# Performance work log

Hardware: AMD Instinct MI355X
Metric: run time of the kernel (lower is better)

## Reference

```python
import jax, jax.numpy as jnp
import numpy as np

N = 100000      # nodes
E = 1600000     # edges (avg degree 16)
D_IN, D_H, D_OUT = 128, 128, 64


def setup_inputs() -> dict:
    key = jax.random.key(0)
    ks = jax.random.split(key, 8)
    x = jax.random.normal(ks[0], (N, D_IN), dtype=jnp.float32)
    edge_index = jax.random.randint(ks[1], (2, E), 0, N, dtype=jnp.int64)

    def lin(k, fi, fo):
        s = float(1.0 / np.sqrt(fi))
        return jax.random.normal(k, (fi, fo), dtype=jnp.float32) * s

    return {
        "x": x,
        "edge_index": edge_index,
        "W0": lin(ks[2], D_IN, D_H),  "b0": jnp.zeros((D_H,), jnp.float32),
        "W1": lin(ks[3], D_H, D_H),   "b1": jnp.zeros((D_H,), jnp.float32),
        "W2": lin(ks[4], D_H, D_OUT), "b2": jnp.zeros((D_OUT,), jnp.float32),
    }


def gcn_conv(x, W, b, src, dst, deg_inv_sqrt):
    # PyG GCNConv: h = x W; out = D^-1/2 (A + I) D^-1/2 h + b
    h = x @ W                                             # [N, F_out]
    coef = deg_inv_sqrt[src] * deg_inv_sqrt[dst]          # [E]
    msg = h[src] * coef[:, None]                          # [E, F_out] gather
    out = jax.ops.segment_sum(msg, dst, num_segments=N)   # scatter-add
    out = out + (deg_inv_sqrt * deg_inv_sqrt)[:, None] * h  # self-loops
    return out + b


def reference(x, edge_index, W0, b0, W1, b1, W2, b2):
    src, dst = edge_index[0], edge_index[1]
    # degree includes the self-loop (+1), matching add_self_loops fill_value=1
    deg = jnp.zeros((N,), x.dtype).at[dst].add(1.0) + 1.0
    dis = jax.lax.rsqrt(deg)

    h = jax.nn.relu(gcn_conv(x, W0, b0, src, dst, dis))   # dropout: eval mode -> identity
    h = jax.nn.relu(gcn_conv(h, W1, b1, src, dst, dis))
    h = gcn_conv(h, W2, b2, src, dst, dis)
    return jax.nn.log_softmax(h, axis=1)
```

## Files before the change

### kernel.cpp

```cpp
#include <hip/hip_runtime.h>
#include <cstddef>

#define NN 100000
#define NE 1600000
#define CB_SH 9
#define NCB ((NN + 511) >> CB_SH)
#define BIN_D 32
#define CAP 8960
#define SORT_D CAP
#define SC_BLOCKS 800
#define RPT 18

typedef unsigned int uint;
typedef unsigned short ushort;
typedef short bf16x8 __attribute__((ext_vector_type(8)));
typedef float f32x16 __attribute__((ext_vector_type(16)));

__device__ inline uint bf16_rne(float f) {
  uint u = __float_as_uint(f);
  u += 0x7fffu + ((u >> 16) & 1u);
  return u >> 16;
}
__device__ inline float blo(uint u) { return __uint_as_float(u << 16); }
__device__ inline float bhi(uint u) { return __uint_as_float(u & 0xffff0000u); }

__global__ void __launch_bounds__(256) k_setup(const float* __restrict__ W0,
                                               const float* __restrict__ W1,
                                               const float* __restrict__ W2,
                                               ushort* __restrict__ W0b,
                                               ushort* __restrict__ W1b,
                                               ushort* __restrict__ W2b,
                                               int* __restrict__ gcur) {
  int b = blockIdx.x, t = threadIdx.x;
  if (b == 3) {
    if (t < NCB) gcur[t] = 0;
    return;
  }
  const float* W = (b == 0) ? W0 : (b == 1) ? W1 : W2;
  ushort* Wb = (b == 0) ? W0b : (b == 1) ? W1b : W2b;
  int FOUT = (b == 2) ? 64 : 128;
  for (int lin = t; lin < 128 * FOUT; lin += 256) {
    int k = lin / FOUT, n = lin % FOUT;
    int c = n >> 5, kc = k >> 4, khi = (k >> 3) & 1, j = k & 7;
    int ln = khi * 32 + (n & 31);
    Wb[(((c * 8 + kc) * 64) + ln) * 8 + j] = (ushort)bf16_rne(W[lin]);
  }
}

__global__ void __launch_bounds__(256) k_binA(const int* __restrict__ src,
                                              const int* __restrict__ dst,
                                              int* __restrict__ gcur,
                                              uint* __restrict__ ebuf, int E) {
  __shared__ uint bins[NCB][BIN_D + 1];
  __shared__ uint bcnt[NCB];
  int t = threadIdx.x;
  for (int j = t; j < NCB; j += 256) bcnt[j] = 0;
  const int per = (E + SC_BLOCKS - 1) / SC_BLOCKS;
  int e0 = blockIdx.x * per, e1 = min(E, e0 + per);
  __syncthreads();
  #pragma unroll
  for (int r = 0; r < 8; ++r) {
    int i = e0 + r * 256 + t;
    if (i < e1) {
      uint s = (uint)src[i], d = (uint)dst[i];
      uint b = d >> CB_SH;
      uint rec = s | ((d & 511u) << 17);
      uint slot = atomicAdd(&bcnt[b], 1u);
      if (slot < BIN_D) bins[b][slot] = rec;
      else ebuf[(size_t)b * CAP + atomicAdd(&gcur[b], 1)] = rec;
    }
  }
  __syncthreads();
  if (t < NCB) {
    uint c = bcnt[t]; if (c > BIN_D) c = BIN_D;
    if (c) {
      int base = atomicAdd(&gcur[t], (int)c);
      for (uint i = 0; i < c; ++i) ebuf[(size_t)t * CAP + base + i] = bins[t][i];
    }
  }
}

__global__ void __launch_bounds__(512) k_csr(const uint* __restrict__ ebuf,
                                             const int* __restrict__ gcur,
                                             int* __restrict__ row_ptr,
                                             float* __restrict__ dis,
                                             uint* __restrict__ edges, int N, int E) {
  __shared__ uint sbuf[SORT_D];
  __shared__ uint c[512];
  __shared__ uint wsum[8];
  int b = blockIdx.x, t = threadIdx.x, lane = t & 63, wv = t >> 6;
  c[t] = 0;

  uint v = (t < b) ? (uint)gcur[t] : 0u;
  #pragma unroll
  for (int d = 32; d; d >>= 1) v += __shfl_xor(v, d, 64);
  if (lane == 0) wsum[wv] = v;
  __syncthreads();
  uint ebase = 0;
  #pragma unroll
  for (int j = 0; j < 8; ++j) ebase += wsum[j];

  int cntb = gcur[b];
  const uint* __restrict__ eb = ebuf + (size_t)b * CAP;
  uint rec[RPT];
  #pragma unroll
  for (int j = 0; j < RPT; ++j) {
    int i = t + j * 512;
    rec[j] = (i < cntb) ? eb[i] : 0xffffffffu;
  }
  #pragma unroll
  for (int j = 0; j < RPT; ++j)
    if (rec[j] != 0xffffffffu) atomicAdd(&c[rec[j] >> 17], 1u);
  __syncthreads();

  uint deg = c[t];
  uint x = deg;
  #pragma unroll
  for (int d = 1; d < 64; d <<= 1) {
    uint y = __shfl_up(x, (uint)d, 64);
    if (lane >= d) x += y;
  }
  if (lane == 63) wsum[wv] = x;
  __syncthreads();
  uint wexcl = 0;
  for (int j = 0; j < wv; ++j) wexcl += wsum[j];
  uint excl = wexcl + (x - deg);

  int g = (b << CB_SH) + t;
  if (g < N) {
    row_ptr[g] = (int)(ebase + excl);
    dis[g] = rsqrtf((float)deg + 1.0f);
  }
  if (b == 0 && t == 0) row_ptr[N] = E;

  c[t] = excl;
  __syncthreads();
  #pragma unroll
  for (int j = 0; j < RPT; ++j)
    if (rec[j] != 0xffffffffu) {
      int pos = atomicAdd(&c[rec[j] >> 17], 1u);
      sbuf[pos] = rec[j] & 0x1ffffu;
    }
  __syncthreads();
  for (int i = t; i < cntb; i += 512)
    edges[ebase + i] = sbuf[i];
}

template <int FOUT, bool BF16IN>
__global__ void __launch_bounds__(512) k_gemm(const void* __restrict__ Xv,
                                              const ushort* __restrict__ Wb,
                                              const float* __restrict__ dis,
                                              ushort* __restrict__ Hb, int M) {
  constexpr int NCT = FOUT / 32;
  constexpr int TPW = NCT / 2;
  __shared__ alignas(16) ushort Af[4 * 8 * 64 * 8];
  __shared__ alignas(16) ushort Wf[NCT * 8 * 64 * 8];
  __shared__ float diss[128];
  int t = threadIdx.x, lane = t & 63, wv = t >> 6;
  int m0 = blockIdx.x * 128;

  if (t < 128) {
    int gm = m0 + t;
    diss[t] = (gm < M) ? dis[gm] : 0.f;
  }
  {
    int m = t >> 2;
    int gm = m0 + m;
    int rb = m >> 5, ml = m & 31;
    #pragma unroll
    for (int i = 0; i < 4; ++i) {
      int g = (t & 3) + i * 4;
      uint4 p = make_uint4(0u, 0u, 0u, 0u);
      if (gm < M) {
        if (BF16IN) {
          const ushort* X = (const ushort*)Xv;
          p = *reinterpret_cast<const uint4*>(X + (size_t)gm * 128 + g * 8);
        } else {
          const float* X = (const float*)Xv;
          float4 va = *reinterpret_cast<const float4*>(X + (size_t)gm * 128 + g * 8);
          float4 vb = *reinterpret_cast<const float4*>(X + (size_t)gm * 128 + g * 8 + 4);
          p.x = bf16_rne(va.x) | (bf16_rne(va.y) << 16);
          p.y = bf16_rne(va.z) | (bf16_rne(va.w) << 16);
          p.z = bf16_rne(vb.x) | (bf16_rne(vb.y) << 16);
          p.w = bf16_rne(vb.z) | (bf16_rne(vb.w) << 16);
        }
      }
      int kc = g >> 1, khi = g & 1;
      int ln = khi * 32 + ml;
      *reinterpret_cast<uint4*>(&Af[(((rb * 8 + kc) * 64) + ln) * 8]) = p;
    }
  }
  {
    constexpr int WU4 = 128 * FOUT * 2 / 16;
    #pragma unroll
    for (int it = 0; it < WU4 / 512; ++it) {
      int idx = it * 512 + t;
      reinterpret_cast<uint4*>(Wf)[idx] = reinterpret_cast<const uint4*>(Wb)[idx];
    }
  }
  __syncthreads();

  f32x16 acc[TPW];
  #pragma unroll
  for (int tp = 0; tp < TPW; ++tp)
    #pragma unroll
    for (int r = 0; r < 16; ++r) acc[tp][r] = 0.f;

  int rb = wv & 3, cg = wv >> 2;
  #pragma unroll
  for (int kc = 0; kc < 8; ++kc) {
    bf16x8 a = *reinterpret_cast<bf16x8*>(&Af[((rb * 8 + kc) * 64 + lane) * 8]);
    #pragma unroll
    for (int tp = 0; tp < TPW; ++tp) {
      int c = cg * TPW + tp;
      bf16x8 bb = *reinterpret_cast<bf16x8*>(&Wf[((c * 8 + kc) * 64 + lane) * 8]);
      acc[tp] = __builtin_amdgcn_mfma_f32_32x32x16_bf16(a, bb, acc[tp], 0, 0, 0);
    }
  }

  #pragma unroll
  for (int tp = 0; tp < TPW; ++tp) {
    int col = (cg * TPW + tp) * 32 + (lane & 31);
    #pragma unroll
    for (int reg = 0; reg < 16; ++reg) {
      int lr = rb * 32 + 4 * (lane >> 5) + (reg & 3) + 8 * (reg >> 2);
      int row = m0 + lr;
      if (row < M) Hb[(size_t)row * FOUT + col] = (ushort)bf16_rne(acc[tp][reg] * diss[lr]);
    }
  }
}

__global__ void __launch_bounds__(256) k_agg128(const uint* __restrict__ hb,
                                                const int* __restrict__ row_ptr,
                                                const uint* __restrict__ edges,
                                                const float* __restrict__ dis,
                                                const float* __restrict__ bias,
                                                uint* __restrict__ outb, int N) {
  int t = threadIdx.x;
  int lane = t & 63, wv = t >> 6;
  int g16 = lane >> 4;
  int sl = lane & 15;
  int gbase = lane & 48;
  int n = blockIdx.x * 16 + wv * 4 + g16;
  if (n >= N) return;
  const uint4* __restrict__ h4 = reinterpret_cast<const uint4*>(hb);
  int beg = row_ptr[n], end = row_ptr[n + 1];

  float acc[8];
  #pragma unroll
  for (int k = 0; k < 8; ++k) acc[k] = 0.f;

  int p = beg;
  for (; p + 8 <= end; p += 8) {
    uint r = edges[p + (lane & 7)];
    uint4 v[8];
    #pragma unroll
    for (int s = 0; s < 8; ++s) {
      uint rec = __shfl(r, gbase + s, 64);
      v[s] = h4[(size_t)rec * 16 + sl];
    }
    #pragma unroll
    for (int s = 0; s < 8; ++s) {
      acc[0] += blo(v[s].x);
      acc[1] += bhi(v[s].x);
      acc[2] += blo(v[s].y);
      acc[3] += bhi(v[s].y);
      acc[4] += blo(v[s].z);
      acc[5] += bhi(v[s].z);
      acc[6] += blo(v[s].w);
      acc[7] += bhi(v[s].w);
    }
  }
  if (p < end) {
    int idx = p + (lane & 7);
    uint r = (idx < end) ? edges[idx] : 0u;
    #pragma unroll
    for (int s = 0; s < 8; ++s) {
      if (p + s < end) {
        uint rec = __shfl(r, gbase + s, 64);
        uint4 v = h4[(size_t)rec * 16 + sl];
        acc[0] += blo(v.x);
        acc[1] += bhi(v.x);
        acc[2] += blo(v.y);
        acc[3] += bhi(v.y);
        acc[4] += blo(v.z);
        acc[5] += bhi(v.z);
        acc[6] += blo(v.w);
        acc[7] += bhi(v.w);
      }
    }
  }

  float dn = dis[n];
  uint4 hv = h4[(size_t)n * 16 + sl];
  const float4* b4 = reinterpret_cast<const float4*>(bias);
  float4 ba = b4[sl * 2], bb2 = b4[sl * 2 + 1];
  float o0 = fmaxf((acc[0] + blo(hv.x)) * dn + ba.x, 0.f);
  float o1 = fmaxf((acc[1] + bhi(hv.x)) * dn + ba.y, 0.f);
  float o2 = fmaxf((acc[2] + blo(hv.y)) * dn + ba.z, 0.f);
  float o3 = fmaxf((acc[3] + bhi(hv.y)) * dn + ba.w, 0.f);
  float o4 = fmaxf((acc[4] + blo(hv.z)) * dn + bb2.x, 0.f);
  float o5 = fmaxf((acc[5] + bhi(hv.z)) * dn + bb2.y, 0.f);
  float o6 = fmaxf((acc[6] + blo(hv.w)) * dn + bb2.z, 0.f);
  float o7 = fmaxf((acc[7] + bhi(hv.w)) * dn + bb2.w, 0.f);
  uint4 pb;
  pb.x = bf16_rne(o0) | (bf16_rne(o1) << 16);
  pb.y = bf16_rne(o2) | (bf16_rne(o3) << 16);
  pb.z = bf16_rne(o4) | (bf16_rne(o5) << 16);
  pb.w = bf16_rne(o6) | (bf16_rne(o7) << 16);
  reinterpret_cast<uint4*>(outb)[(size_t)n * 16 + sl] = pb;
}

__global__ void __launch_bounds__(256) k_agg64(const uint* __restrict__ hb,
                                               const int* __restrict__ row_ptr,
                                               const uint* __restrict__ edges,
                                               const float* __restrict__ dis,
                                               const float* __restrict__ bias,
                                               float* __restrict__ out, int N) {
  int t = threadIdx.x;
  int lane = t & 63, wv = t >> 6;
  int g8 = lane >> 3;
  int sl = lane & 7;
  int gbase = lane & 56;
  int n = blockIdx.x * 32 + wv * 8 + g8;
  if (n >= N) return;
  const uint4* __restrict__ h4 = reinterpret_cast<const uint4*>(hb);
  int beg = row_ptr[n], end = row_ptr[n + 1];

  float acc[8];
  #pragma unroll
  for (int k = 0; k < 8; ++k) acc[k] = 0.f;

  int p = beg;
  for (; p + 8 <= end; p += 8) {
    uint r = edges[p + sl];
    uint4 v[8];
    #pragma unroll
    for (int s = 0; s < 8; ++s) {
      uint rec = __shfl(r, gbase + s, 64);
      v[s] = h4[(size_t)rec * 8 + sl];
    }
    #pragma unroll
    for (int s = 0; s < 8; ++s) {
      acc[0] += blo(v[s].x);
      acc[1] += bhi(v[s].x);
      acc[2] += blo(v[s].y);
      acc[3] += bhi(v[s].y);
      acc[4] += blo(v[s].z);
      acc[5] += bhi(v[s].z);
      acc[6] += blo(v[s].w);
      acc[7] += bhi(v[s].w);
    }
  }
  if (p < end) {
    int idx = p + sl;
    uint r = (idx < end) ? edges[idx] : 0u;
    #pragma unroll
    for (int s = 0; s < 8; ++s) {
      if (p + s < end) {
        uint rec = __shfl(r, gbase + s, 64);
        uint4 v = h4[(size_t)rec * 8 + sl];
        acc[0] += blo(v.x);
        acc[1] += bhi(v.x);
        acc[2] += blo(v.y);
        acc[3] += bhi(v.y);
        acc[4] += blo(v.z);
        acc[5] += bhi(v.z);
        acc[6] += blo(v.w);
        acc[7] += bhi(v.w);
      }
    }
  }

  float dn = dis[n];
  uint4 hv = h4[(size_t)n * 8 + sl];
  const float4* b4 = reinterpret_cast<const float4*>(bias);
  float4 ba = b4[sl * 2], bb2 = b4[sl * 2 + 1];
  float z[8];
  z[0] = (acc[0] + blo(hv.x)) * dn + ba.x;
  z[1] = (acc[1] + bhi(hv.x)) * dn + ba.y;
  z[2] = (acc[2] + blo(hv.y)) * dn + ba.z;
  z[3] = (acc[3] + bhi(hv.y)) * dn + ba.w;
  z[4] = (acc[4] + blo(hv.z)) * dn + bb2.x;
  z[5] = (acc[5] + bhi(hv.z)) * dn + bb2.y;
  z[6] = (acc[6] + blo(hv.w)) * dn + bb2.z;
  z[7] = (acc[7] + bhi(hv.w)) * dn + bb2.w;

  float m = z[0];
  #pragma unroll
  for (int k = 1; k < 8; ++k) m = fmaxf(m, z[k]);
  m = fmaxf(m, __shfl_xor(m, 1, 64));
  m = fmaxf(m, __shfl_xor(m, 2, 64));
  m = fmaxf(m, __shfl_xor(m, 4, 64));
  float e = 0.f;
  #pragma unroll
  for (int k = 0; k < 8; ++k) e += __expf(z[k] - m);
  e += __shfl_xor(e, 1, 64);
  e += __shfl_xor(e, 2, 64);
  e += __shfl_xor(e, 4, 64);
  float lse = m + __logf(e);

  float4* orow = reinterpret_cast<float4*>(out + (size_t)n * 64);
  orow[sl * 2]     = make_float4(z[0] - lse, z[1] - lse, z[2] - lse, z[3] - lse);
  orow[sl * 2 + 1] = make_float4(z[4] - lse, z[5] - lse, z[6] - lse, z[7] - lse);
}

extern "C" void kernel_launch(void* const* d_in, const int* in_sizes, int n_in,
                              void* d_out, int out_size, void* d_ws, size_t ws_size,
                              hipStream_t stream) {
  const float* x  = (const float*)d_in[0];
  const int*   ei = (const int*)d_in[1];
  const float* W0 = (const float*)d_in[2];
  const float* b0 = (const float*)d_in[3];
  const float* W1 = (const float*)d_in[4];
  const float* b1 = (const float*)d_in[5];
  const float* W2 = (const float*)d_in[6];
  const float* b2 = (const float*)d_in[7];
  float* out = (float*)d_out;

  const int N = NN, E = NE;
  const int* src = ei;
  const int* dst = ei + E;

  char* ws = (char*)d_ws;
  size_t off = 0;
  auto alloc = [&](size_t bytes) -> void* {
    off = (off + 255) & ~(size_t)255;
    void* p = ws + off;
    off += bytes;
    return p;
  };
  float*  dis     = (float*)alloc((size_t)N * 4);
  int*    row_ptr = (int*)alloc((size_t)(N + 1) * 4);
  int*    gcur    = (int*)alloc((size_t)NCB * 4);
  uint*   ebuf    = (uint*)alloc((size_t)NCB * CAP * 4);
  uint*   edges   = (uint*)alloc((size_t)E * 4);
  ushort* bufAb   = (ushort*)alloc((size_t)N * 128 * 2);
  ushort* bufBb   = (ushort*)alloc((size_t)N * 128 * 2);
  ushort* W0b     = (ushort*)alloc(128 * 128 * 2);
  ushort* W1b     = (ushort*)alloc(128 * 128 * 2);
  ushort* W2b     = (ushort*)alloc(128 * 64 * 2);

  k_setup<<<4, 256, 0, stream>>>(W0, W1, W2, W0b, W1b, W2b, gcur);
  k_binA<<<SC_BLOCKS, 256, 0, stream>>>(src, dst, gcur, ebuf, E);
  k_csr<<<NCB, 512, 0, stream>>>(ebuf, gcur, row_ptr, dis, edges, N, E);

  const int gemm_grid = (N + 127) / 128;
  const int agg128_grid = (N + 15) / 16;
  const int agg64_grid = (N + 31) / 32;

  k_gemm<128, false><<<gemm_grid, 512, 0, stream>>>(x, W0b, dis, bufAb, N);
  k_agg128<<<agg128_grid, 256, 0, stream>>>((const uint*)bufAb, row_ptr, edges, dis, b0, (uint*)bufBb, N);
  k_gemm<128, true><<<gemm_grid, 512, 0, stream>>>(bufBb, W1b, dis, bufAb, N);
  k_agg128<<<agg128_grid, 256, 0, stream>>>((const uint*)bufAb, row_ptr, edges, dis, b1, (uint*)bufBb, N);
  k_gemm<64, true><<<gemm_grid, 512, 0, stream>>>(bufBb, W2b, dis, bufAb, N);
  k_agg64<<<agg64_grid, 256, 0, stream>>>((const uint*)bufAb, row_ptr, edges, dis, b2, out, N);
}
```

Baseline: 338.9 us.

## Fuse weight setup, edge binning and CSR build into one cooperative kernel

Replaces the three graph-preprocessing launches (weight conversion, edge binning, CSR sort) with a single cooperative kernel that separates the phases with grid-wide syncs. The binning phase now runs on 512 persistent blocks of 512 threads, each looping over its edge range in chunks and flushing its LDS bins after every chunk. The aim is to remove launch overhead and inter-kernel gaps. In exchange it adds two grid barriers, depends on all 512 blocks being co-resident, and flushes the partial bins more often.

```diff
diff --git a/kernel.cpp b/kernel.cpp
--- a/kernel.cpp
+++ b/kernel.cpp
@@ -1,5 +1,8 @@
 #include <hip/hip_runtime.h>
+#include <hip/hip_cooperative_groups.h>
 #include <cstddef>
+
+namespace cg = cooperative_groups;
 
 #define NN 100000
 #define NE 1600000
@@ -8,8 +11,8 @@
 #define BIN_D 32
 #define CAP 8960
 #define SORT_D CAP
-#define SC_BLOCKS 800
 #define RPT 18
+#define BLD_BLOCKS 512
 
 typedef unsigned int uint;
 typedef unsigned short ushort;
@@ -24,126 +27,135 @@
 __device__ inline float blo(uint u) { return __uint_as_float(u << 16); }
 __device__ inline float bhi(uint u) { return __uint_as_float(u & 0xffff0000u); }
 
-__global__ void __launch_bounds__(256) k_setup(const float* __restrict__ W0,
-                                               const float* __restrict__ W1,
-                                               const float* __restrict__ W2,
-                                               ushort* __restrict__ W0b,
-                                               ushort* __restrict__ W1b,
-                                               ushort* __restrict__ W2b,
-                                               int* __restrict__ gcur) {
-  int b = blockIdx.x, t = threadIdx.x;
-  if (b == 3) {
+__global__ void __launch_bounds__(512, 4) k_build(const float* __restrict__ W0,
+                                                  const float* __restrict__ W1,
+                                                  const float* __restrict__ W2,
+                                                  ushort* __restrict__ W0b,
+                                                  ushort* __restrict__ W1b,
+                                                  ushort* __restrict__ W2b,
+                                                  const int* __restrict__ src,
+                                                  const int* __restrict__ dst,
+                                                  int* __restrict__ gcur,
+                                                  uint* __restrict__ ebuf,
+                                                  int* __restrict__ row_ptr,
+                                                  float* __restrict__ dis,
+                                                  uint* __restrict__ edges,
+                                                  int N, int E) {
+  __shared__ uint lds[SORT_D + 512 + 8];
+  cg::grid_group grid = cg::this_grid();
+  int blk = blockIdx.x, t = threadIdx.x, lane = t & 63, wv = t >> 6;
+
+  if (blk == 3) {
     if (t < NCB) gcur[t] = 0;
-    return;
-  }
-  const float* W = (b == 0) ? W0 : (b == 1) ? W1 : W2;
-  ushort* Wb = (b == 0) ? W0b : (b == 1) ? W1b : W2b;
-  int FOUT = (b == 2) ? 64 : 128;
-  for (int lin = t; lin < 128 * FOUT; lin += 256) {
-    int k = lin / FOUT, n = lin % FOUT;
-    int c = n >> 5, kc = k >> 4, khi = (k >> 3) & 1, j = k & 7;
-    int ln = khi * 32 + (n & 31);
-    Wb[(((c * 8 + kc) * 64) + ln) * 8 + j] = (ushort)bf16_rne(W[lin]);
-  }
-}
-
-__global__ void __launch_bounds__(256) k_binA(const int* __restrict__ src,
-                                              const int* __restrict__ dst,
-                                              int* __restrict__ gcur,
-                                              uint* __restrict__ ebuf, int E) {
-  __shared__ uint bins[NCB][BIN_D + 1];
-  __shared__ uint bcnt[NCB];
-  int t = threadIdx.x;
-  for (int j = t; j < NCB; j += 256) bcnt[j] = 0;
-  const int per = (E + SC_BLOCKS - 1) / SC_BLOCKS;
-  int e0 = blockIdx.x * per, e1 = min(E, e0 + per);
-  __syncthreads();
-  #pragma unroll
-  for (int r = 0; r < 8; ++r) {
-    int i = e0 + r * 256 + t;
-    if (i < e1) {
-      uint s = (uint)src[i], d = (uint)dst[i];
-      uint b = d >> CB_SH;
-      uint rec = s | ((d & 511u) << 17);
-      uint slot = atomicAdd(&bcnt[b], 1u);
-      if (slot < BIN_D) bins[b][slot] = rec;
-      else ebuf[(size_t)b * CAP + atomicAdd(&gcur[b], 1)] = rec;
-    }
-  }
-  __syncthreads();
-  if (t < NCB) {
-    uint c = bcnt[t]; if (c > BIN_D) c = BIN_D;
-    if (c) {
-      int base = atomicAdd(&gcur[t], (int)c);
-      for (uint i = 0; i < c; ++i) ebuf[(size_t)t * CAP + base + i] = bins[t][i];
-    }
-  }
-}
-
-__global__ void __launch_bounds__(512) k_csr(const uint* __restrict__ ebuf,
-                                             const int* __restrict__ gcur,
-                                             int* __restrict__ row_ptr,
-                                             float* __restrict__ dis,
-                                             uint* __restrict__ edges, int N, int E) {
-  __shared__ uint sbuf[SORT_D];
-  __shared__ uint c[512];
-  __shared__ uint wsum[8];
-  int b = blockIdx.x, t = threadIdx.x, lane = t & 63, wv = t >> 6;
-  c[t] = 0;
-
-  uint v = (t < b) ? (uint)gcur[t] : 0u;
-  #pragma unroll
-  for (int d = 32; d; d >>= 1) v += __shfl_xor(v, d, 64);
-  if (lane == 0) wsum[wv] = v;
-  __syncthreads();
-  uint ebase = 0;
-  #pragma unroll
-  for (int j = 0; j < 8; ++j) ebase += wsum[j];
-
-  int cntb = gcur[b];
-  const uint* __restrict__ eb = ebuf + (size_t)b * CAP;
-  uint rec[RPT];
-  #pragma unroll
-  for (int j = 0; j < RPT; ++j) {
-    int i = t + j * 512;
-    rec[j] = (i < cntb) ? eb[i] : 0xffffffffu;
-  }
-  #pragma unroll
-  for (int j = 0; j < RPT; ++j)
-    if (rec[j] != 0xffffffffu) atomicAdd(&c[rec[j] >> 17], 1u);
-  __syncthreads();
-
-  uint deg = c[t];
-  uint x = deg;
-  #pragma unroll
-  for (int d = 1; d < 64; d <<= 1) {
-    uint y = __shfl_up(x, (uint)d, 64);
-    if (lane >= d) x += y;
-  }
-  if (lane == 63) wsum[wv] = x;
-  __syncthreads();
-  uint wexcl = 0;
-  for (int j = 0; j < wv; ++j) wexcl += wsum[j];
-  uint excl = wexcl + (x - deg);
-
-  int g = (b << CB_SH) + t;
-  if (g < N) {
-    row_ptr[g] = (int)(ebase + excl);
-    dis[g] = rsqrtf((float)deg + 1.0f);
-  }
-  if (b == 0 && t == 0) row_ptr[N] = E;
-
-  c[t] = excl;
-  __syncthreads();
-  #pragma unroll
-  for (int j = 0; j < RPT; ++j)
-    if (rec[j] != 0xffffffffu) {
-      int pos = atomicAdd(&c[rec[j] >> 17], 1u);
-      sbuf[pos] = rec[j] & 0x1ffffu;
-    }
-  __syncthreads();
-  for (int i = t; i < cntb; i += 512)
-    edges[ebase + i] = sbuf[i];
+  } else if (blk < 3) {
+    const float* W = (blk == 0) ? W0 : (blk == 1) ? W1 : W2;
+    ushort* Wb = (blk == 0) ? W0b : (blk == 1) ? W1b : W2b;
+    int FOUT = (blk == 2) ? 64 : 128;
+    for (int lin = t; lin < 128 * FOUT; lin += 512) {
+      int k = lin / FOUT, n = lin % FOUT;
+      int c = n >> 5, kc = k >> 4, khi = (k >> 3) & 1, j = k & 7;
+      int ln = khi * 32 + (n & 31);
+      Wb[(((c * 8 + kc) * 64) + ln) * 8 + j] = (ushort)bf16_rne(W[lin]);
+    }
+  }
+  grid.sync();
+
+  {
+    uint (*bins)[BIN_D + 1] = reinterpret_cast<uint (*)[BIN_D + 1]>(lds);
+    uint* bcnt = lds + NCB * (BIN_D + 1);
+    for (int j = t; j < NCB; j += 512) bcnt[j] = 0;
+    const int per = (E + BLD_BLOCKS - 1) / BLD_BLOCKS;
+    int e0 = blk * per, e1 = min(E, e0 + per);
+    __syncthreads();
+    for (int rb = e0; rb < e1; rb += 2048) {
+      #pragma unroll
+      for (int r = 0; r < 4; ++r) {
+        int i = rb + r * 512 + t;
+        if (i < e1 && i < rb + 2048) {
+          uint s = (uint)src[i], d = (uint)dst[i];
+          uint b = d >> CB_SH;
+          uint rec = s | ((d & 511u) << 17);
+          uint slot = atomicAdd(&bcnt[b], 1u);
+          if (slot < BIN_D) bins[b][slot] = rec;
+          else ebuf[(size_t)b * CAP + atomicAdd(&gcur[b], 1)] = rec;
+        }
+      }
+      __syncthreads();
+      if (t < NCB) {
+        uint c = bcnt[t]; if (c > BIN_D) c = BIN_D;
+        if (c) {
+          int base = atomicAdd(&gcur[t], (int)c);
+          for (uint i = 0; i < c; ++i) ebuf[(size_t)t * CAP + base + i] = bins[t][i];
+        }
+        bcnt[t] = 0;
+      }
+      __syncthreads();
+    }
+  }
+  grid.sync();
+
+  if (blk < NCB) {
+    uint* sbuf = lds;
+    uint* c = lds + SORT_D;
+    uint* wsum = lds + SORT_D + 512;
+    int b = blk;
+    c[t] = 0;
+
+    uint v = (t < b) ? (uint)gcur[t] : 0u;
+    #pragma unroll
+    for (int d = 32; d; d >>= 1) v += __shfl_xor(v, d, 64);
+    if (lane == 0) wsum[wv] = v;
+    __syncthreads();
+    uint ebase = 0;
+    #pragma unroll
+    for (int j = 0; j < 8; ++j) ebase += wsum[j];
+
+    int cntb = gcur[b];
+    const uint* __restrict__ eb = ebuf + (size_t)b * CAP;
+    uint rec[RPT];
+    #pragma unroll
+    for (int j = 0; j < RPT; ++j) {
+      int i = t + j * 512;
+      rec[j] = (i < cntb) ? eb[i] : 0xffffffffu;
+    }
+    #pragma unroll
+    for (int j = 0; j < RPT; ++j)
+      if (rec[j] != 0xffffffffu) atomicAdd(&c[rec[j] >> 17], 1u);
+    __syncthreads();
+
+    uint deg = c[t];
+    uint x = deg;
+    #pragma unroll
+    for (int d = 1; d < 64; d <<= 1) {
+      uint y = __shfl_up(x, (uint)d, 64);
+      if (lane >= d) x += y;
+    }
+    if (lane == 63) wsum[wv] = x;
+    __syncthreads();
+    uint wexcl = 0;
+    for (int j = 0; j < wv; ++j) wexcl += wsum[j];
+    uint excl = wexcl + (x - deg);
+
+    int g = (b << CB_SH) + t;
+    if (g < N) {
+      row_ptr[g] = (int)(ebase + excl);
+      dis[g] = rsqrtf((float)deg + 1.0f);
+    }
+    if (b == 0 && t == 0) row_ptr[N] = E;
+
+    __syncthreads();
+    c[t] = excl;
+    __syncthreads();
+    #pragma unroll
+    for (int j = 0; j < RPT; ++j)
+      if (rec[j] != 0xffffffffu) {
+        int pos = atomicAdd(&c[rec[j] >> 17], 1u);
+        sbuf[pos] = rec[j] & 0x1ffffu;
+      }
+    __syncthreads();
+    for (int i = t; i < cntb; i += 512)
+      edges[ebase + i] = sbuf[i];
+  }
 }
 
 template <int FOUT, bool BF16IN>
@@ -206,13 +218,13 @@
     #pragma unroll
     for (int r = 0; r < 16; ++r) acc[tp][r] = 0.f;
 
-  int rb = wv & 3, cg = wv >> 2;
+  int rb = wv & 3, cg2 = wv >> 2;
   #pragma unroll
   for (int kc = 0; kc < 8; ++kc) {
     bf16x8 a = *reinterpret_cast<bf16x8*>(&Af[((rb * 8 + kc) * 64 + lane) * 8]);
     #pragma unroll
     for (int tp = 0; tp < TPW; ++tp) {
-      int c = cg * TPW + tp;
+      int c = cg2 * TPW + tp;
       bf16x8 bb = *reinterpret_cast<bf16x8*>(&Wf[((c * 8 + kc) * 64 + lane) * 8]);
       acc[tp] = __builtin_amdgcn_mfma_f32_32x32x16_bf16(a, bb, acc[tp], 0, 0, 0);
     }
@@ -220,7 +232,7 @@
 
   #pragma unroll
   for (int tp = 0; tp < TPW; ++tp) {
-    int col = (cg * TPW + tp) * 32 + (lane & 31);
+    int col = (cg2 * TPW + tp) * 32 + (lane & 31);
     #pragma unroll
     for (int reg = 0; reg < 16; ++reg) {
       int lr = rb * 32 + 4 * (lane >> 5) + (reg & 3) + 8 * (reg >> 2);
@@ -418,7 +430,7 @@
   const float* b2 = (const float*)d_in[7];
   float* out = (float*)d_out;
 
-  const int N = NN, E = NE;
+  int N = NN, E = NE;
   const int* src = ei;
   const int* dst = ei + E;
 
@@ -441,9 +453,16 @@
   ushort* W1b     = (ushort*)alloc(128 * 128 * 2);
   ushort* W2b     = (ushort*)alloc(128 * 64 * 2);
 
-  k_setup<<<4, 256, 0, stream>>>(W0, W1, W2, W0b, W1b, W2b, gcur);
-  k_binA<<<SC_BLOCKS, 256, 0, stream>>>(src, dst, gcur, ebuf, E);
-  k_csr<<<NCB, 512, 0, stream>>>(ebuf, gcur, row_ptr, dis, edges, N, E);
+  {
+    void* args[] = {(void*)&W0, (void*)&W1, (void*)&W2,
+                    (void*)&W0b, (void*)&W1b, (void*)&W2b,
+                    (void*)&src, (void*)&dst,
+                    (void*)&gcur, (void*)&ebuf,
+                    (void*)&row_ptr, (void*)&dis, (void*)&edges,
+                    (void*)&N, (void*)&E};
+    hipLaunchCooperativeKernel((void*)k_build, dim3(BLD_BLOCKS), dim3(512),
+                               args, 0, stream);
+  }
 
   const int gemm_grid = (N + 127) / 128;
   const int agg128_grid = (N + 15) / 16;
```

Result: slower. 447.0 us (+31.9%).
